# Kernel tuning notes

Measured on AMD Instinct MI355X. Metric: run time of the kernel, lower is better.

Reference implementation:

```python
import jax, jax.numpy as jnp
import numpy as np

HEAD_DIM = 64  # config['head_dim']
# dropout_prob=0.1 is a no-op in eval mode; reference computes deterministic attention.

def setup_inputs() -> dict:
    key = jax.random.key(0)
    kq, kk, kv = jax.random.split(key, 3)
    shape = (2, 12, 2048, HEAD_DIM)  # [batch, heads, seq, head_dim]
    Q = jax.random.normal(kq, shape, dtype=jnp.float32)
    K = jax.random.normal(kk, shape, dtype=jnp.float32)
    V = jax.random.normal(kv, shape, dtype=jnp.float32)
    return {"Q": Q, "K": K, "V": V}

def reference(Q, K, V):
    # dot = Q @ K^T / sqrt(head_dim); attn = softmax(dot); X = attn @ V
    scale = 1.0 / np.float32(np.sqrt(HEAD_DIM))
    dot = jnp.einsum('bhqd,bhkd->bhqk', Q, K) * scale  # [B,H,S,S]
    attn = jax.nn.softmax(dot, axis=-1)
    X = jnp.einsum('bhqk,bhkd->bhqd', attn, V)
    return X
```

## Files before the change

### kernel.cpp

```cpp
#include <hip/hip_runtime.h>
#include <hip/hip_bf16.h>

typedef __attribute__((ext_vector_type(8))) short bf16x8;
typedef __attribute__((ext_vector_type(4))) float f32x4;
typedef __attribute__((ext_vector_type(4))) unsigned short u16x4;
typedef __attribute__((ext_vector_type(2))) unsigned int u32x2;
typedef __attribute__((ext_vector_type(4))) unsigned int u32x4;
typedef __attribute__((ext_vector_type(4))) _Float16 f16x4;
typedef __attribute__((ext_vector_type(8))) _Float16 f16x8;
typedef __attribute__((ext_vector_type(2))) __fp16 h16x2;
typedef __attribute__((ext_vector_type(4))) __fp16 h16x4;

#define SEQ 2048
#define HD 64
#define BH 24

__device__ __forceinline__ unsigned bfpack(float a, float b) {
  union { float f; unsigned u; } ua, ub; ua.f = a; ub.f = b;
  return __builtin_amdgcn_perm(ub.u + 0x8000u, ua.u + 0x8000u, 0x07060302u);
}
__device__ __forceinline__ unsigned short f2bf(float f) {
  union { float f; unsigned u; } v; v.f = f;
  unsigned r = v.u + 0x7fffu + ((v.u >> 16) & 1u);
  return (unsigned short)(r >> 16);
}

__global__ __launch_bounds__(256) void prep_kv(const float* __restrict__ K,
                                               const float* __restrict__ V,
                                               unsigned* __restrict__ Kb,
                                               _Float16* __restrict__ Vt) {
  __shared__ _Float16 t[64 * 68];
  const int bh = blockIdx.y;
  const int k0 = blockIdx.x * 64;
  const int tid = threadIdx.x;

  const float4* ks = (const float4*)(K + ((size_t)bh * SEQ + k0) * HD);
  unsigned* kd = Kb + ((size_t)bh * SEQ + k0) * (HD / 2);
#pragma unroll
  for (int i = 0; i < 4; ++i) {
    int f = tid + i * 256;
    float4 v = ks[f];
    u32x2 o;
    o.x = bfpack(v.x, v.y);
    o.y = bfpack(v.z, v.w);
    *(u32x2*)&kd[f * 2] = o;
  }

  const float4* vs = (const float4*)(V + ((size_t)bh * SEQ + k0) * HD);
#pragma unroll
  for (int i = 0; i < 4; ++i) {
    int f = tid + i * 256;
    int k = f >> 4, cg = f & 15;
    float4 v = vs[k * 16 + cg];
    int dg = cg * 4;
    t[(dg + 0) * 68 + k] = (_Float16)v.x;
    t[(dg + 1) * 68 + k] = (_Float16)v.y;
    t[(dg + 2) * 68 + k] = (_Float16)v.z;
    t[(dg + 3) * 68 + k] = (_Float16)v.w;
  }
  __syncthreads();
  int d = tid >> 2, kg = (tid & 3) * 16;
  _Float16* g = Vt + ((size_t)(bh * 64 + d)) * SEQ + k0 + kg;
#pragma unroll
  for (int r = 0; r < 4; ++r) {
    f16x4 x = *(f16x4*)&t[d * 68 + kg + r * 4];
    *(f16x4*)&g[r * 4] = x;
  }
}

__global__ __launch_bounds__(256, 3) void attn_main(const float* __restrict__ Q,
                                                    const unsigned short* __restrict__ Kb,
                                                    const _Float16* __restrict__ Vt,
                                                    float* __restrict__ O) {
  __shared__ unsigned short kv[3][8192];

  const int tid  = threadIdx.x;
  const int lane = tid & 63;
  const int w    = tid >> 6;
  const int quad = lane >> 4;
  const int n    = lane & 15;

  const int bh = blockIdx.x;
  const int q0 = blockIdx.y * 64;

  const float qscale = 0.125f * 1.44269504088896f;

  bf16x8 qf[4][2];
#pragma unroll
  for (int u = 0; u < 4; ++u) {
    const float* qb = Q + ((size_t)bh * SEQ + q0 + u * 16 + n) * HD;
#pragma unroll
    for (int h = 0; h < 2; ++h) {
      float4 a = *(const float4*)(qb + h * 32 + quad * 8);
      float4 b = *(const float4*)(qb + h * 32 + quad * 8 + 4);
      u32x4 pk;
      pk.x = bfpack(a.x * qscale, a.y * qscale);
      pk.y = bfpack(a.z * qscale, a.w * qscale);
      pk.z = bfpack(b.x * qscale, b.y * qscale);
      pk.w = bfpack(b.z * qscale, b.w * qscale);
      qf[u][h] = __builtin_bit_cast(bf16x8, pk);
    }
  }

  const unsigned short* Kbase = Kb + (size_t)bh * SEQ * HD;
  const unsigned short* Vbase = (const unsigned short*)(Vt + (size_t)bh * HD * SEQ);
  const unsigned short* ksrc[2];
  const unsigned short* vsrc[2];
  int soff[2];
#pragma unroll
  for (int i = 0; i < 2; ++i) {
    int s = i * 256 + tid;
    int r = s >> 3, p = s & 7, G = p ^ (r & 7);
    ksrc[i] = Kbase + r * HD + G * 8;
    vsrc[i] = Vbase + (size_t)r * SEQ + G * 8;
    soff[i] = s * 8;
  }

#define DMA_TO(buf_, it_)                                                                 \
  {                                                                                       \
    unsigned short* db_ = &kv[buf_][0];                                                   \
    _Pragma("unroll")                                                                     \
    for (int i_ = 0; i_ < 2; ++i_) {                                                      \
      __builtin_amdgcn_global_load_lds(                                                   \
          (const __attribute__((address_space(1))) void*)(ksrc[i_] + (size_t)(it_) * 4096), \
          (__attribute__((address_space(3))) void*)(db_ + soff[i_]), 16, 0, 0);           \
      __builtin_amdgcn_global_load_lds(                                                   \
          (const __attribute__((address_space(1))) void*)(vsrc[i_] + (size_t)(it_) * 64), \
          (__attribute__((address_space(3))) void*)(db_ + 4096 + soff[i_]), 16, 0, 0);    \
    }                                                                                     \
    asm volatile("" ::: "memory");                                                        \
  }

  f32x4 o[4][4];
#pragma unroll
  for (int dt = 0; dt < 4; ++dt)
#pragma unroll
    for (int u = 0; u < 4; ++u) o[dt][u] = (f32x4){0.f, 0.f, 0.f, 0.f};
  float lsum[4] = {0.f, 0.f, 0.f, 0.f};

  int ro[2];
#pragma unroll
  for (int h = 0; h < 2; ++h) ro[h] = n * 64 + (((h * 4 + quad) ^ (n & 7)) * 8);
  int vo[4];
#pragma unroll
  for (int dt = 0; dt < 4; ++dt)
    vo[dt] = dt * 1024 + n * 64 + (((w * 2 + (quad >> 1)) ^ (n & 7)) * 8) + (quad & 1) * 4;

#define COMPUTE(buf_)                                                                     \
  {                                                                                       \
    const unsigned short* kb = &kv[buf_][0];                                              \
    const unsigned short* vb = kb + 4096;                                                 \
    f32x4 s[4] = {{0,0,0,0},{0,0,0,0},{0,0,0,0},{0,0,0,0}};                               \
    _Pragma("unroll")                                                                     \
    for (int h = 0; h < 2; ++h) {                                                         \
      bf16x8 a = *(const bf16x8*)&kb[w * 1024 + ro[h]];                                   \
      _Pragma("unroll")                                                                   \
      for (int u = 0; u < 4; ++u)                                                         \
        s[u] = __builtin_amdgcn_mfma_f32_16x16x32_bf16(a, qf[u][h], s[u], 0, 0, 0);       \
    }                                                                                     \
    f16x4 pf[4];                                                                          \
    _Pragma("unroll")                                                                     \
    for (int u = 0; u < 4; ++u) {                                                         \
      float e0 = __builtin_amdgcn_exp2f(s[u][0]);                                         \
      float e1 = __builtin_amdgcn_exp2f(s[u][1]);                                         \
      float e2 = __builtin_amdgcn_exp2f(s[u][2]);                                         \
      float e3 = __builtin_amdgcn_exp2f(s[u][3]);                                         \
      lsum[u] += (e0 + e1) + (e2 + e3);                                                   \
      h16x2 a_ = __builtin_amdgcn_cvt_pkrtz(e0, e1);                                      \
      h16x2 b_ = __builtin_amdgcn_cvt_pkrtz(e2, e3);                                      \
      h16x4 ab_ = __builtin_shufflevector(a_, b_, 0, 1, 2, 3);                            \
      pf[u] = __builtin_bit_cast(f16x4, ab_);                                             \
    }                                                                                     \
    _Pragma("unroll")                                                                     \
    for (int dt = 0; dt < 4; ++dt) {                                                      \
      f16x4 vf = *(const f16x4*)((const _Float16*)vb + vo[dt]);                           \
      _Pragma("unroll")                                                                   \
      for (int u = 0; u < 4; ++u)                                                         \
        o[dt][u] = __builtin_amdgcn_mfma_f32_16x16x16f16(vf, pf[u], o[dt][u], 0, 0, 0);   \
    }                                                                                     \
  }

  DMA_TO(0, 0);
  DMA_TO(1, 1);

  int bc = 0;
  int bd = 2;
  for (int it = 0; it < 31; ++it) {
    asm volatile("s_waitcnt vmcnt(4)\n\ts_barrier" ::: "memory");
    if (it < 30) DMA_TO(bd, it + 2);
    COMPUTE(bc);
    bc = (bc == 2) ? 0 : bc + 1;
    bd = (bd == 2) ? 0 : bd + 1;
  }
  asm volatile("s_waitcnt vmcnt(0)\n\ts_barrier" ::: "memory");
  COMPUTE(bc);

#undef DMA_TO
#undef COMPUTE

#pragma unroll
  for (int u = 0; u < 4; ++u) {
    lsum[u] += __shfl_xor(lsum[u], 16);
    lsum[u] += __shfl_xor(lsum[u], 32);
  }

  float* red = (float*)&kv[0][0];
  float* lred = red + 2 * 4096;

  __syncthreads();
  if (w & 1) {
    int s = w >> 1;
#pragma unroll
    for (int dt = 0; dt < 4; ++dt)
#pragma unroll
      for (int u = 0; u < 4; ++u)
        *(f32x4*)&red[s * 4096 + (dt * 4 + u) * 256 + lane * 4] = o[dt][u];
#pragma unroll
    for (int u = 0; u < 4; ++u) lred[s * 256 + u * 64 + lane] = lsum[u];
  }
  __syncthreads();
  if (!(w & 1)) {
    int s = w >> 1;
#pragma unroll
    for (int dt = 0; dt < 4; ++dt)
#pragma unroll
      for (int u = 0; u < 4; ++u)
        o[dt][u] += *(f32x4*)&red[s * 4096 + (dt * 4 + u) * 256 + lane * 4];
#pragma unroll
    for (int u = 0; u < 4; ++u) lsum[u] += lred[s * 256 + u * 64 + lane];
  }
  __syncthreads();
  if (w == 2) {
#pragma unroll
    for (int dt = 0; dt < 4; ++dt)
#pragma unroll
      for (int u = 0; u < 4; ++u)
        *(f32x4*)&red[4096 + (dt * 4 + u) * 256 + lane * 4] = o[dt][u];
#pragma unroll
    for (int u = 0; u < 4; ++u) lred[256 + u * 64 + lane] = lsum[u];
  }
  __syncthreads();
  if (w == 0) {
#pragma unroll
    for (int dt = 0; dt < 4; ++dt)
#pragma unroll
      for (int u = 0; u < 4; ++u)
        o[dt][u] += *(f32x4*)&red[4096 + (dt * 4 + u) * 256 + lane * 4];
#pragma unroll
    for (int u = 0; u < 4; ++u) {
      float inv = 1.0f / (lsum[u] + lred[256 + u * 64 + lane]);
      float* og = O + ((size_t)bh * SEQ + q0 + u * 16 + n) * HD + quad * 4;
#pragma unroll
      for (int dt = 0; dt < 4; ++dt) {
        f32x4 r = o[dt][u];
        r.x *= inv; r.y *= inv; r.z *= inv; r.w *= inv;
        *(f32x4*)(og + dt * 16) = r;
      }
    }
  }
}

#define F_QT 128
#define F_KT 64
#define F_LD 72

__global__ __launch_bounds__(512) void attn_fwd(const float* __restrict__ Q,
                                                const float* __restrict__ K,
                                                const float* __restrict__ V,
                                                float* __restrict__ O) {
  __shared__ unsigned short sm[(F_QT + F_KT + HD + 8 * 16) * F_LD];
  unsigned short* Qs = sm;
  unsigned short* Ks = Qs + F_QT * F_LD;
  unsigned short* Vt = Ks + F_KT * F_LD;
  unsigned short* Ps = Vt + HD * F_LD;

  const int tid = threadIdx.x, lane = tid & 63, wv = tid >> 6;
  const int quad = lane >> 4, n = lane & 15;
  const int bh = blockIdx.y, q0 = blockIdx.x * F_QT;
  const float* Qg = Q + ((size_t)bh * SEQ + q0) * HD;
  const float* Kg = K + (size_t)bh * SEQ * HD;
  const float* Vg = V + (size_t)bh * SEQ * HD;
  float* Og = O + ((size_t)bh * SEQ + q0) * HD;
  const float qscale = 0.125f * 1.44269504088896f;

#pragma unroll
  for (int i = 0; i < 4; ++i) {
    int f = tid + i * 512;
    int row = f >> 4, cg = f & 15;
    float4 qv = ((const float4*)Qg)[row * 16 + cg];
    u16x4 h;
    h.x = f2bf(qv.x * qscale); h.y = f2bf(qv.y * qscale);
    h.z = f2bf(qv.z * qscale); h.w = f2bf(qv.w * qscale);
    *(u16x4*)&Qs[row * F_LD + cg * 4] = h;
  }
  __syncthreads();
  bf16x8 qf0 = *(const bf16x8*)&Qs[(wv * 16 + n) * F_LD + quad * 8];
  bf16x8 qf1 = *(const bf16x8*)&Qs[(wv * 16 + n) * F_LD + 32 + quad * 8];
  f32x4 o[4] = {{0,0,0,0},{0,0,0,0},{0,0,0,0},{0,0,0,0}};
  float mrow[4] = {-1e30f,-1e30f,-1e30f,-1e30f};
  float lrow[4] = {0.f,0.f,0.f,0.f};
  unsigned short* Pw = Ps + wv * 16 * F_LD;

  for (int it = 0; it < SEQ / F_KT; ++it) {
    __syncthreads();
    const float* Ktg = Kg + (size_t)it * F_KT * HD;
    const float* Vtg = Vg + (size_t)it * F_KT * HD;
#pragma unroll
    for (int i = 0; i < 2; ++i) {
      int f = tid + i * 512;
      int row = f >> 4, cg = f & 15;
      float4 kvv = ((const float4*)Ktg)[row * 16 + cg];
      u16x4 hk;
      hk.x = f2bf(kvv.x); hk.y = f2bf(kvv.y); hk.z = f2bf(kvv.z); hk.w = f2bf(kvv.w);
      *(u16x4*)&Ks[row * F_LD + cg * 4] = hk;
      float4 vv = ((const float4*)Vtg)[row * 16 + cg];
      Vt[(cg * 4 + 0) * F_LD + row] = f2bf(vv.x);
      Vt[(cg * 4 + 1) * F_LD + row] = f2bf(vv.y);
      Vt[(cg * 4 + 2) * F_LD + row] = f2bf(vv.z);
      Vt[(cg * 4 + 3) * F_LD + row] = f2bf(vv.w);
    }
    __syncthreads();
    f32x4 s[4];
#pragma unroll
    for (int t = 0; t < 4; ++t) {
      bf16x8 b0 = *(const bf16x8*)&Ks[(t * 16 + n) * F_LD + quad * 8];
      bf16x8 b1 = *(const bf16x8*)&Ks[(t * 16 + n) * F_LD + 32 + quad * 8];
      f32x4 c = {0,0,0,0};
      c = __builtin_amdgcn_mfma_f32_16x16x32_bf16(qf0, b0, c, 0, 0, 0);
      c = __builtin_amdgcn_mfma_f32_16x16x32_bf16(qf1, b1, c, 0, 0, 0);
      s[t] = c;
    }
    float mnew[4], alpha[4], rsum[4];
#pragma unroll
    for (int r = 0; r < 4; ++r) {
      float ml = fmaxf(fmaxf(s[0][r], s[1][r]), fmaxf(s[2][r], s[3][r]));
      ml = fmaxf(ml, __shfl_xor(ml, 1));
      ml = fmaxf(ml, __shfl_xor(ml, 2));
      ml = fmaxf(ml, __shfl_xor(ml, 4));
      ml = fmaxf(ml, __shfl_xor(ml, 8));
      mnew[r] = fmaxf(mrow[r], ml);
      alpha[r] = __builtin_amdgcn_exp2f(mrow[r] - mnew[r]);
      mrow[r] = mnew[r];
      rsum[r] = 0.f;
    }
#pragma unroll
    for (int t = 0; t < 4; ++t)
#pragma unroll
      for (int r = 0; r < 4; ++r) {
        float p = __builtin_amdgcn_exp2f(s[t][r] - mnew[r]);
        rsum[r] += p;
        Pw[(quad * 4 + r) * F_LD + t * 16 + n] = f2bf(p);
      }
#pragma unroll
    for (int r = 0; r < 4; ++r) {
      float rs = rsum[r];
      rs += __shfl_xor(rs, 1); rs += __shfl_xor(rs, 2);
      rs += __shfl_xor(rs, 4); rs += __shfl_xor(rs, 8);
      lrow[r] = lrow[r] * alpha[r] + rs;
      o[0][r] *= alpha[r]; o[1][r] *= alpha[r];
      o[2][r] *= alpha[r]; o[3][r] *= alpha[r];
    }
    asm volatile("s_waitcnt lgkmcnt(0)" ::: "memory");
    bf16x8 p0 = *(const bf16x8*)&Pw[n * F_LD + quad * 8];
    bf16x8 p1 = *(const bf16x8*)&Pw[n * F_LD + 32 + quad * 8];
#pragma unroll
    for (int t = 0; t < 4; ++t) {
      bf16x8 v0 = *(const bf16x8*)&Vt[(t * 16 + n) * F_LD + quad * 8];
      bf16x8 v1 = *(const bf16x8*)&Vt[(t * 16 + n) * F_LD + 32 + quad * 8];
      o[t] = __builtin_amdgcn_mfma_f32_16x16x32_bf16(p0, v0, o[t], 0, 0, 0);
      o[t] = __builtin_amdgcn_mfma_f32_16x16x32_bf16(p1, v1, o[t], 0, 0, 0);
    }
  }
  float inv[4];
#pragma unroll
  for (int r = 0; r < 4; ++r) inv[r] = 1.0f / lrow[r];
#pragma unroll
  for (int t = 0; t < 4; ++t)
#pragma unroll
    for (int r = 0; r < 4; ++r)
      Og[(wv * 16 + quad * 4 + r) * HD + t * 16 + n] = o[t][r] * inv[r];
}

extern "C" void kernel_launch(void* const* d_in, const int* in_sizes, int n_in,
                              void* d_out, int out_size, void* d_ws, size_t ws_size,
                              hipStream_t stream) {
  const float* Q = (const float*)d_in[0];
  const float* K = (const float*)d_in[1];
  const float* V = (const float*)d_in[2];
  float* O = (float*)d_out;

  const size_t mat = (size_t)BH * SEQ * HD;
  const size_t need = 2 * mat * sizeof(unsigned short);

  if (ws_size >= need) {
    unsigned short* Kb = (unsigned short*)d_ws;
    _Float16* Vt = (_Float16*)(Kb + mat);
    prep_kv<<<dim3(SEQ / 64, BH), 256, 0, stream>>>(K, V, (unsigned*)Kb, Vt);
    attn_main<<<dim3(BH, SEQ / 64), 256, 0, stream>>>(Q, Kb, Vt, O);
  } else {
    attn_fwd<<<dim3(SEQ / F_QT, BH), 512, 0, stream>>>(Q, K, V, O);
  }
}
```

Baseline: 119.5 us.

## Split attention block into 8 waves over query halves and key quarters

Each block of the main attention kernel now uses 512 threads (8 waves) instead of 256. Waves are arranged as 2 query halves by 4 key slices, so each wave holds half as many query fragments and accumulators. The DMA per thread drops to one K and one V chunk per tile, and the wait count and the cross-wave reduction are adjusted to match. The goal is more waves per CU and lower register pressure, which should hide latency better. The cost is that K/V fragments loaded from LDS are reused across fewer query rows, and synchronisation covers more waves.

```diff
diff --git a/kernel.cpp b/kernel.cpp
--- a/kernel.cpp
+++ b/kernel.cpp
@@ -68,7 +68,7 @@
   }
 }
 
-__global__ __launch_bounds__(256, 3) void attn_main(const float* __restrict__ Q,
+__global__ __launch_bounds__(512, 5) void attn_main(const float* __restrict__ Q,
                                                     const unsigned short* __restrict__ Kb,
                                                     const _Float16* __restrict__ Vt,
                                                     float* __restrict__ O) {
@@ -77,6 +77,8 @@
   const int tid  = threadIdx.x;
   const int lane = tid & 63;
   const int w    = tid >> 6;
+  const int kq   = w & 3;
+  const int qh   = w >> 2;
   const int quad = lane >> 4;
   const int n    = lane & 15;
 
@@ -85,10 +87,10 @@
 
   const float qscale = 0.125f * 1.44269504088896f;
 
-  bf16x8 qf[4][2];
-#pragma unroll
-  for (int u = 0; u < 4; ++u) {
-    const float* qb = Q + ((size_t)bh * SEQ + q0 + u * 16 + n) * HD;
+  bf16x8 qf[2][2];
+#pragma unroll
+  for (int u = 0; u < 2; ++u) {
+    const float* qb = Q + ((size_t)bh * SEQ + q0 + qh * 32 + u * 16 + n) * HD;
 #pragma unroll
     for (int h = 0; h < 2; ++h) {
       float4 a = *(const float4*)(qb + h * 32 + quad * 8);
@@ -104,63 +106,54 @@
 
   const unsigned short* Kbase = Kb + (size_t)bh * SEQ * HD;
   const unsigned short* Vbase = (const unsigned short*)(Vt + (size_t)bh * HD * SEQ);
-  const unsigned short* ksrc[2];
-  const unsigned short* vsrc[2];
-  int soff[2];
-#pragma unroll
-  for (int i = 0; i < 2; ++i) {
-    int s = i * 256 + tid;
-    int r = s >> 3, p = s & 7, G = p ^ (r & 7);
-    ksrc[i] = Kbase + r * HD + G * 8;
-    vsrc[i] = Vbase + (size_t)r * SEQ + G * 8;
-    soff[i] = s * 8;
-  }
+  const int r_ = tid >> 3, p_ = tid & 7, G_ = p_ ^ (r_ & 7);
+  const unsigned short* ksrc = Kbase + r_ * HD + G_ * 8;
+  const unsigned short* vsrc = Vbase + (size_t)r_ * SEQ + G_ * 8;
+  const int soff = tid * 8;
 
 #define DMA_TO(buf_, it_)                                                                 \
   {                                                                                       \
     unsigned short* db_ = &kv[buf_][0];                                                   \
-    _Pragma("unroll")                                                                     \
-    for (int i_ = 0; i_ < 2; ++i_) {                                                      \
-      __builtin_amdgcn_global_load_lds(                                                   \
-          (const __attribute__((address_space(1))) void*)(ksrc[i_] + (size_t)(it_) * 4096), \
-          (__attribute__((address_space(3))) void*)(db_ + soff[i_]), 16, 0, 0);           \
-      __builtin_amdgcn_global_load_lds(                                                   \
-          (const __attribute__((address_space(1))) void*)(vsrc[i_] + (size_t)(it_) * 64), \
-          (__attribute__((address_space(3))) void*)(db_ + 4096 + soff[i_]), 16, 0, 0);    \
-    }                                                                                     \
+    __builtin_amdgcn_global_load_lds(                                                     \
+        (const __attribute__((address_space(1))) void*)(ksrc + (size_t)(it_) * 4096),     \
+        (__attribute__((address_space(3))) void*)(db_ + soff), 16, 0, 0);                 \
+    __builtin_amdgcn_global_load_lds(                                                     \
+        (const __attribute__((address_space(1))) void*)(vsrc + (size_t)(it_) * 64),       \
+        (__attribute__((address_space(3))) void*)(db_ + 4096 + soff), 16, 0, 0);          \
     asm volatile("" ::: "memory");                                                        \
   }
 
-  f32x4 o[4][4];
+  f32x4 o[4][2];
 #pragma unroll
   for (int dt = 0; dt < 4; ++dt)
 #pragma unroll
-    for (int u = 0; u < 4; ++u) o[dt][u] = (f32x4){0.f, 0.f, 0.f, 0.f};
-  float lsum[4] = {0.f, 0.f, 0.f, 0.f};
+    for (int u = 0; u < 2; ++u) o[dt][u] = (f32x4){0.f, 0.f, 0.f, 0.f};
+  float lsum[2] = {0.f, 0.f};
 
   int ro[2];
 #pragma unroll
-  for (int h = 0; h < 2; ++h) ro[h] = n * 64 + (((h * 4 + quad) ^ (n & 7)) * 8);
+  for (int h = 0; h < 2; ++h)
+    ro[h] = (kq * 16 + n) * 64 + (((h * 4 + quad) ^ (n & 7)) * 8);
   int vo[4];
 #pragma unroll
   for (int dt = 0; dt < 4; ++dt)
-    vo[dt] = dt * 1024 + n * 64 + (((w * 2 + (quad >> 1)) ^ (n & 7)) * 8) + (quad & 1) * 4;
+    vo[dt] = (dt * 16 + n) * 64 + (((kq * 2 + (quad >> 1)) ^ (n & 7)) * 8) + (quad & 1) * 4;
 
 #define COMPUTE(buf_)                                                                     \
   {                                                                                       \
     const unsigned short* kb = &kv[buf_][0];                                              \
     const unsigned short* vb = kb + 4096;                                                 \
-    f32x4 s[4] = {{0,0,0,0},{0,0,0,0},{0,0,0,0},{0,0,0,0}};                               \
+    f32x4 s[2] = {{0,0,0,0},{0,0,0,0}};                                                   \
     _Pragma("unroll")                                                                     \
     for (int h = 0; h < 2; ++h) {                                                         \
-      bf16x8 a = *(const bf16x8*)&kb[w * 1024 + ro[h]];                                   \
+      bf16x8 a = *(const bf16x8*)&kb[ro[h]];                                              \
       _Pragma("unroll")                                                                   \
-      for (int u = 0; u < 4; ++u)                                                         \
+      for (int u = 0; u < 2; ++u)                                                         \
         s[u] = __builtin_amdgcn_mfma_f32_16x16x32_bf16(a, qf[u][h], s[u], 0, 0, 0);       \
     }                                                                                     \
-    f16x4 pf[4];                                                                          \
+    f16x4 pf[2];                                                                          \
     _Pragma("unroll")                                                                     \
-    for (int u = 0; u < 4; ++u) {                                                         \
+    for (int u = 0; u < 2; ++u) {                                                         \
       float e0 = __builtin_amdgcn_exp2f(s[u][0]);                                         \
       float e1 = __builtin_amdgcn_exp2f(s[u][1]);                                         \
       float e2 = __builtin_amdgcn_exp2f(s[u][2]);                                         \
@@ -175,7 +168,7 @@
     for (int dt = 0; dt < 4; ++dt) {                                                      \
       f16x4 vf = *(const f16x4*)((const _Float16*)vb + vo[dt]);                           \
       _Pragma("unroll")                                                                   \
-      for (int u = 0; u < 4; ++u)                                                         \
+      for (int u = 0; u < 2; ++u)                                                         \
         o[dt][u] = __builtin_amdgcn_mfma_f32_16x16x16f16(vf, pf[u], o[dt][u], 0, 0, 0);   \
     }                                                                                     \
   }
@@ -186,7 +179,7 @@
   int bc = 0;
   int bd = 2;
   for (int it = 0; it < 31; ++it) {
-    asm volatile("s_waitcnt vmcnt(4)\n\ts_barrier" ::: "memory");
+    asm volatile("s_waitcnt vmcnt(2)\n\ts_barrier" ::: "memory");
     if (it < 30) DMA_TO(bd, it + 2);
     COMPUTE(bc);
     bc = (bc == 2) ? 0 : bc + 1;
@@ -199,57 +192,57 @@
 #undef COMPUTE
 
 #pragma unroll
-  for (int u = 0; u < 4; ++u) {
+  for (int u = 0; u < 2; ++u) {
     lsum[u] += __shfl_xor(lsum[u], 16);
     lsum[u] += __shfl_xor(lsum[u], 32);
   }
 
   float* red = (float*)&kv[0][0];
-  float* lred = red + 2 * 4096;
-
-  __syncthreads();
-  if (w & 1) {
-    int s = w >> 1;
+  float* lred = red + 4 * 2048;
+
+  __syncthreads();
+  if (kq >= 2) {
+    int slot = qh * 2 + (kq - 2);
 #pragma unroll
     for (int dt = 0; dt < 4; ++dt)
 #pragma unroll
-      for (int u = 0; u < 4; ++u)
-        *(f32x4*)&red[s * 4096 + (dt * 4 + u) * 256 + lane * 4] = o[dt][u];
-#pragma unroll
-    for (int u = 0; u < 4; ++u) lred[s * 256 + u * 64 + lane] = lsum[u];
-  }
-  __syncthreads();
-  if (!(w & 1)) {
-    int s = w >> 1;
+      for (int u = 0; u < 2; ++u)
+        *(f32x4*)&red[slot * 2048 + (dt * 2 + u) * 256 + lane * 4] = o[dt][u];
+#pragma unroll
+    for (int u = 0; u < 2; ++u) lred[slot * 128 + u * 64 + lane] = lsum[u];
+  }
+  __syncthreads();
+  if (kq < 2) {
+    int slot = qh * 2 + kq;
 #pragma unroll
     for (int dt = 0; dt < 4; ++dt)
 #pragma unroll
-      for (int u = 0; u < 4; ++u)
-        o[dt][u] += *(f32x4*)&red[s * 4096 + (dt * 4 + u) * 256 + lane * 4];
-#pragma unroll
-    for (int u = 0; u < 4; ++u) lsum[u] += lred[s * 256 + u * 64 + lane];
-  }
-  __syncthreads();
-  if (w == 2) {
+      for (int u = 0; u < 2; ++u)
+        o[dt][u] += *(f32x4*)&red[slot * 2048 + (dt * 2 + u) * 256 + lane * 4];
+#pragma unroll
+    for (int u = 0; u < 2; ++u) lsum[u] += lred[slot * 128 + u * 64 + lane];
+  }
+  __syncthreads();
+  if (kq == 1) {
 #pragma unroll
     for (int dt = 0; dt < 4; ++dt)
 #pragma unroll
-      for (int u = 0; u < 4; ++u)
-        *(f32x4*)&red[4096 + (dt * 4 + u) * 256 + lane * 4] = o[dt][u];
-#pragma unroll
-    for (int u = 0; u < 4; ++u) lred[256 + u * 64 + lane] = lsum[u];
-  }
-  __syncthreads();
-  if (w == 0) {
-#pragma unroll
-    for (int dt = 0; dt < 4; ++dt)
-#pragma unroll
-      for (int u = 0; u < 4; ++u)
-        o[dt][u] += *(f32x4*)&red[4096 + (dt * 4 + u) * 256 + lane * 4];
-#pragma unroll
-    for (int u = 0; u < 4; ++u) {
-      float inv = 1.0f / (lsum[u] + lred[256 + u * 64 + lane]);
-      float* og = O + ((size_t)bh * SEQ + q0 + u * 16 + n) * HD + quad * 4;
+      for (int u = 0; u < 2; ++u)
+        *(f32x4*)&red[qh * 2048 + (dt * 2 + u) * 256 + lane * 4] = o[dt][u];
+#pragma unroll
+    for (int u = 0; u < 2; ++u) lred[qh * 128 + u * 64 + lane] = lsum[u];
+  }
+  __syncthreads();
+  if (kq == 0) {
+#pragma unroll
+    for (int u = 0; u < 2; ++u) {
+      float ltot = lsum[u];
+#pragma unroll
+      for (int dt = 0; dt < 4; ++dt)
+        o[dt][u] += *(f32x4*)&red[qh * 2048 + (dt * 2 + u) * 256 + lane * 4];
+      ltot += lred[qh * 128 + u * 64 + lane];
+      float inv = 1.0f / ltot;
+      float* og = O + ((size_t)bh * SEQ + q0 + qh * 32 + u * 16 + n) * HD + quad * 4;
 #pragma unroll
       for (int dt = 0; dt < 4; ++dt) {
         f32x4 r = o[dt][u];
@@ -396,7 +389,7 @@
     unsigned short* Kb = (unsigned short*)d_ws;
     _Float16* Vt = (_Float16*)(Kb + mat);
     prep_kv<<<dim3(SEQ / 64, BH), 256, 0, stream>>>(K, V, (unsigned*)Kb, Vt);
-    attn_main<<<dim3(BH, SEQ / 64), 256, 0, stream>>>(Q, Kb, Vt, O);
+    attn_main<<<dim3(BH, SEQ / 64), 512, 0, stream>>>(Q, Kb, Vt, O);
   } else {
     attn_fwd<<<dim3(SEQ / F_QT, BH), 512, 0, stream>>>(Q, K, V, O);
   }
```

Measured after the change: 119.9 us. No clear change (+0.4%).

## Give each wave private LDS buffers and drop per-iteration block barriers

Applied to the files above, without the earlier changes.

Each wave now loads only its own 16-key slice of K and V into a private triple-buffered LDS region, with a new swizzle, instead of the whole block sharing one 64-key tile. Because no wave reads another wave's data, the per-iteration s_barrier is removed and each wave waits only on its own vmcnt. The DMA for the next tile is issued before the wait, and the V fragments are hoisted ahead of the softmax. This removes block-wide synchronisation stalls and lets waves drift apart, but it relies on each wave's own vmcnt being enough to see its own LDS writes without a barrier.

```diff
diff --git a/kernel.cpp b/kernel.cpp
--- a/kernel.cpp
+++ b/kernel.cpp
@@ -72,11 +72,11 @@
                                                     const unsigned short* __restrict__ Kb,
                                                     const _Float16* __restrict__ Vt,
                                                     float* __restrict__ O) {
-  __shared__ unsigned short kv[3][8192];
+  __shared__ unsigned char lds[4][3][4096];
 
   const int tid  = threadIdx.x;
   const int lane = tid & 63;
-  const int w    = tid >> 6;
+  const int kq   = tid >> 6;
   const int quad = lane >> 4;
   const int n    = lane & 15;
 
@@ -106,27 +106,30 @@
   const unsigned short* Vbase = (const unsigned short*)(Vt + (size_t)bh * HD * SEQ);
   const unsigned short* ksrc[2];
   const unsigned short* vsrc[2];
-  int soff[2];
+  int kdst[2], vdst[2];
 #pragma unroll
   for (int i = 0; i < 2; ++i) {
-    int s = i * 256 + tid;
+    int s = i * 64 + lane;
     int r = s >> 3, p = s & 7, G = p ^ (r & 7);
-    ksrc[i] = Kbase + r * HD + G * 8;
-    vsrc[i] = Vbase + (size_t)r * SEQ + G * 8;
-    soff[i] = s * 8;
-  }
+    ksrc[i] = Kbase + (kq * 16 + r) * HD + G * 8;
+    kdst[i] = s * 16;
+    int d = s >> 1, g2 = (s & 1) ^ ((d >> 2) & 1);
+    vsrc[i] = Vbase + (size_t)d * SEQ + kq * 16 + g2 * 8;
+    vdst[i] = 2048 + s * 16;
+  }
+  unsigned char* wbase = &lds[kq][0][0];
 
 #define DMA_TO(buf_, it_)                                                                 \
   {                                                                                       \
-    unsigned short* db_ = &kv[buf_][0];                                                   \
+    unsigned char* db_ = wbase + (buf_) * 4096;                                           \
     _Pragma("unroll")                                                                     \
     for (int i_ = 0; i_ < 2; ++i_) {                                                      \
       __builtin_amdgcn_global_load_lds(                                                   \
           (const __attribute__((address_space(1))) void*)(ksrc[i_] + (size_t)(it_) * 4096), \
-          (__attribute__((address_space(3))) void*)(db_ + soff[i_]), 16, 0, 0);           \
+          (__attribute__((address_space(3))) void*)(db_ + kdst[i_]), 16, 0, 0);           \
       __builtin_amdgcn_global_load_lds(                                                   \
           (const __attribute__((address_space(1))) void*)(vsrc[i_] + (size_t)(it_) * 64), \
-          (__attribute__((address_space(3))) void*)(db_ + 4096 + soff[i_]), 16, 0, 0);    \
+          (__attribute__((address_space(3))) void*)(db_ + vdst[i_]), 16, 0, 0);           \
     }                                                                                     \
     asm volatile("" ::: "memory");                                                        \
   }
@@ -138,26 +141,29 @@
     for (int u = 0; u < 4; ++u) o[dt][u] = (f32x4){0.f, 0.f, 0.f, 0.f};
   float lsum[4] = {0.f, 0.f, 0.f, 0.f};
 
-  int ro[2];
-#pragma unroll
-  for (int h = 0; h < 2; ++h) ro[h] = n * 64 + (((h * 4 + quad) ^ (n & 7)) * 8);
-  int vo[4];
+  int koff[2];
+#pragma unroll
+  for (int h = 0; h < 2; ++h)
+    koff[h] = n * 128 + (((h * 4 + quad) ^ (n & 7)) * 16);
+  int voff[4];
 #pragma unroll
   for (int dt = 0; dt < 4; ++dt)
-    vo[dt] = dt * 1024 + n * 64 + (((w * 2 + (quad >> 1)) ^ (n & 7)) * 8) + (quad & 1) * 4;
+    voff[dt] = 2048 + (dt * 16 + n) * 32 + (((quad >> 1) ^ ((n >> 2) & 1)) * 16) + (quad & 1) * 8;
 
 #define COMPUTE(buf_)                                                                     \
   {                                                                                       \
-    const unsigned short* kb = &kv[buf_][0];                                              \
-    const unsigned short* vb = kb + 4096;                                                 \
+    const unsigned char* kb = wbase + (buf_) * 4096;                                      \
+    bf16x8 a0 = *(const bf16x8*)(kb + koff[0]);                                           \
+    bf16x8 a1 = *(const bf16x8*)(kb + koff[1]);                                           \
     f32x4 s[4] = {{0,0,0,0},{0,0,0,0},{0,0,0,0},{0,0,0,0}};                               \
     _Pragma("unroll")                                                                     \
-    for (int h = 0; h < 2; ++h) {                                                         \
-      bf16x8 a = *(const bf16x8*)&kb[w * 1024 + ro[h]];                                   \
-      _Pragma("unroll")                                                                   \
-      for (int u = 0; u < 4; ++u)                                                         \
-        s[u] = __builtin_amdgcn_mfma_f32_16x16x32_bf16(a, qf[u][h], s[u], 0, 0, 0);       \
+    for (int u = 0; u < 4; ++u) {                                                         \
+      s[u] = __builtin_amdgcn_mfma_f32_16x16x32_bf16(a0, qf[u][0], s[u], 0, 0, 0);        \
+      s[u] = __builtin_amdgcn_mfma_f32_16x16x32_bf16(a1, qf[u][1], s[u], 0, 0, 0);        \
     }                                                                                     \
+    f16x4 vf[4];                                                                          \
+    _Pragma("unroll")                                                                     \
+    for (int dt = 0; dt < 4; ++dt) vf[dt] = *(const f16x4*)(kb + voff[dt]);               \
     f16x4 pf[4];                                                                          \
     _Pragma("unroll")                                                                     \
     for (int u = 0; u < 4; ++u) {                                                         \
@@ -172,12 +178,10 @@
       pf[u] = __builtin_bit_cast(f16x4, ab_);                                             \
     }                                                                                     \
     _Pragma("unroll")                                                                     \
-    for (int dt = 0; dt < 4; ++dt) {                                                      \
-      f16x4 vf = *(const f16x4*)((const _Float16*)vb + vo[dt]);                           \
+    for (int dt = 0; dt < 4; ++dt)                                                        \
       _Pragma("unroll")                                                                   \
       for (int u = 0; u < 4; ++u)                                                         \
-        o[dt][u] = __builtin_amdgcn_mfma_f32_16x16x16f16(vf, pf[u], o[dt][u], 0, 0, 0);   \
-    }                                                                                     \
+        o[dt][u] = __builtin_amdgcn_mfma_f32_16x16x16f16(vf[dt], pf[u], o[dt][u], 0, 0, 0); \
   }
 
   DMA_TO(0, 0);
@@ -185,14 +189,17 @@
 
   int bc = 0;
   int bd = 2;
-  for (int it = 0; it < 31; ++it) {
-    asm volatile("s_waitcnt vmcnt(4)\n\ts_barrier" ::: "memory");
-    if (it < 30) DMA_TO(bd, it + 2);
+  for (int it = 0; it < 30; ++it) {
+    DMA_TO(bd, it + 2);
+    asm volatile("s_waitcnt vmcnt(8)" ::: "memory");
     COMPUTE(bc);
     bc = (bc == 2) ? 0 : bc + 1;
     bd = (bd == 2) ? 0 : bd + 1;
   }
-  asm volatile("s_waitcnt vmcnt(0)\n\ts_barrier" ::: "memory");
+  asm volatile("s_waitcnt vmcnt(4)" ::: "memory");
+  COMPUTE(bc);
+  bc = (bc == 2) ? 0 : bc + 1;
+  asm volatile("s_waitcnt vmcnt(0)" ::: "memory");
   COMPUTE(bc);
 
 #undef DMA_TO
@@ -204,12 +211,12 @@
     lsum[u] += __shfl_xor(lsum[u], 32);
   }
 
-  float* red = (float*)&kv[0][0];
+  float* red = (float*)&lds[0][0][0];
   float* lred = red + 2 * 4096;
 
   __syncthreads();
-  if (w & 1) {
-    int s = w >> 1;
+  if (kq & 1) {
+    int s = kq >> 1;
 #pragma unroll
     for (int dt = 0; dt < 4; ++dt)
 #pragma unroll
@@ -219,8 +226,8 @@
     for (int u = 0; u < 4; ++u) lred[s * 256 + u * 64 + lane] = lsum[u];
   }
   __syncthreads();
-  if (!(w & 1)) {
-    int s = w >> 1;
+  if (!(kq & 1)) {
+    int s = kq >> 1;
 #pragma unroll
     for (int dt = 0; dt < 4; ++dt)
 #pragma unroll
@@ -230,7 +237,7 @@
     for (int u = 0; u < 4; ++u) lsum[u] += lred[s * 256 + u * 64 + lane];
   }
   __syncthreads();
-  if (w == 2) {
+  if (kq == 2) {
 #pragma unroll
     for (int dt = 0; dt < 4; ++dt)
 #pragma unroll
@@ -240,7 +247,7 @@
     for (int u = 0; u < 4; ++u) lred[256 + u * 64 + lane] = lsum[u];
   }
   __syncthreads();
-  if (w == 0) {
+  if (kq == 0) {
 #pragma unroll
     for (int dt = 0; dt < 4; ++dt)
 #pragma unroll
```

After: 122.9 us. +2.9%, slower.
